# Optimization experiments

Measured on AMD Instinct MI355X. Metric: run time of the kernel, lower is better.

The kernel has to match this reference:

```python
import jax, jax.numpy as jnp
import numpy as np

MIN_STD = 0.01
FOURIER_SCALE = 20.0


def _grid_sample_bilinear(h_flat, gx, gy):
    """Bilinear grid_sample with align_corners=True.
    h_flat: (N, C, H, W); gx, gy: (N, P) in [-1, 1].
    Returns (N, P, C)."""
    N, C, H, W = h_flat.shape
    x = (gx + 1.0) * 0.5 * (W - 1)
    y = (gy + 1.0) * 0.5 * (H - 1)
    x0 = jnp.clip(jnp.floor(x), 0, W - 1)
    y0 = jnp.clip(jnp.floor(y), 0, H - 1)
    x1 = jnp.clip(x0 + 1, 0, W - 1)
    y1 = jnp.clip(y0 + 1, 0, H - 1)
    wx = x - x0
    wy = y - y0
    x0i, x1i = x0.astype(jnp.int32), x1.astype(jnp.int32)
    y0i, y1i = y0.astype(jnp.int32), y1.astype(jnp.int32)
    hf = h_flat.reshape(N, C, H * W)  # flatten spatial for gather

    def gather(yi, xi):
        idx = (yi * W + xi)[:, None, :]  # (N,1,P)
        return jnp.take_along_axis(hf, idx, axis=2)  # (N,C,P)

    v00 = gather(y0i, x0i)
    v01 = gather(y0i, x1i)
    v10 = gather(y1i, x0i)
    v11 = gather(y1i, x1i)
    wx_ = wx[:, None, :]
    wy_ = wy[:, None, :]
    top = v00 * (1 - wx_) + v01 * wx_
    bot = v10 * (1 - wx_) + v11 * wx_
    out = top * (1 - wy_) + bot * wy_  # (N,C,P)
    return out.transpose(0, 2, 1)  # (N,P,C)


def setup_inputs() -> dict:
    key = jax.random.key(0)
    ks = jax.random.split(key, 9)
    B, T, C, Hg, Wg, P = 8, 16, 128, 64, 64, 2048
    h_dim, fmap = 128, 128
    in_dim = h_dim + 2 * fmap  # 384
    h_grid = jax.random.normal(ks[0], (B, T, C, Hg, Wg), dtype=jnp.float32)
    xs = jax.random.uniform(ks[1], (B, T, P, 1), dtype=jnp.float32)
    ys = jax.random.uniform(ks[2], (B, T, P, 1), dtype=jnp.float32)
    B_mat = jax.random.normal(ks[3], (2, fmap), dtype=jnp.float32) * FOURIER_SCALE
    W0 = jax.random.normal(ks[4], (in_dim, h_dim), dtype=jnp.float32) / np.sqrt(in_dim)
    b0 = jnp.zeros((h_dim,), dtype=jnp.float32)
    W1 = jax.random.normal(ks[5], (h_dim, h_dim), dtype=jnp.float32) / np.sqrt(h_dim)
    b1 = jnp.zeros((h_dim,), dtype=jnp.float32)
    W2 = jax.random.normal(ks[6], (h_dim, 2), dtype=jnp.float32) / np.sqrt(h_dim)
    b2 = jnp.zeros((2,), dtype=jnp.float32)
    return {"h_grid": h_grid, "xs": xs, "ys": ys, "B_mat": B_mat,
            "W0": W0, "b0": b0, "W1": W1, "b1": b1, "W2": W2, "b2": b2}


def reference(h_grid, xs, ys, B_mat, W0, b0, W1, b1, W2, b2):
    B, T, P, _ = xs.shape
    _, _, C, Hg, Wg = h_grid.shape
    h_flat = h_grid.reshape(B * T, C, Hg, Wg)
    coords = jnp.concatenate([xs, ys], axis=-1).reshape(B * T, P, 2)
    # map [spatial_min, spatial_max]=[0,1] to [-1,1]
    g = 2.0 * coords - 1.0
    sampled = _grid_sample_bilinear(h_flat, g[..., 0], g[..., 1])  # (BT,P,C)
    # Fourier features: [sin(2pi x B), cos(2pi x B)]
    proj = 2.0 * jnp.pi * jnp.einsum('npd,df->npf', coords, B_mat)
    spatial = jnp.concatenate([jnp.sin(proj), jnp.cos(proj)], axis=-1)  # (BT,P,256)
    x = jnp.concatenate([sampled, spatial], axis=-1)  # (BT,P,384)
    x = jax.nn.relu(x @ W0 + b0)
    x = jax.nn.relu(x @ W1 + b1)
    out = (x @ W2 + b2).reshape(B, T, P, 2)
    mu = out[..., 0:1]
    sigma = jax.nn.softplus(out[..., 1:2]) + MIN_STD
    return jnp.concatenate([mu, sigma], axis=-1)  # (B,T,P,2)
```

## Files before the change

### kernel.cpp

```cpp
#include <hip/hip_runtime.h>
#include <hip/hip_bf16.h>
#include <math.h>

typedef __attribute__((ext_vector_type(8))) short short8;
typedef __attribute__((ext_vector_type(4))) float f32x4;
typedef __attribute__((ext_vector_type(4))) unsigned short us4;

#define MFMA_BF16 __builtin_amdgcn_mfma_f32_16x16x32_bf16

__device__ __forceinline__ float b2f(unsigned short u) {
    union { unsigned int i; float f; } v; v.i = ((unsigned int)u) << 16; return v.f;
}
__device__ __forceinline__ unsigned short f2b(float f) {
    __hip_bfloat16 h = __float2bfloat16(f);
    return *reinterpret_cast<unsigned short*>(&h);
}

__global__ __launch_bounds__(256) void transpose_h(const float* __restrict__ hg,
                                                   unsigned short* __restrict__ ht) {
    __shared__ float t[128][65];
    int bid = blockIdx.x;
    int x = bid & 7, r = bid >> 3;
    int n = x * 16 + (r & 15);
    int pb = r >> 4;
    int tid = threadIdx.x;
    const float* src = hg + (size_t)n * 128 * 4096 + pb * 64;
    int j = tid & 63, i0 = tid >> 6;
#pragma unroll
    for (int ii = 0; ii < 32; ++ii) {
        int ch = ii * 4 + i0;
        t[ch][j] = src[(size_t)ch * 4096 + j];
    }
    __syncthreads();
#pragma unroll
    for (int it = 0; it < 8; ++it) {
        int idx = tid + it * 256;
        int px = idx >> 5, cq = idx & 31;
        us4 o;
#pragma unroll
        for (int rr = 0; rr < 4; ++rr) o[rr] = f2b(t[cq * 4 + rr][px]);
        *(us4*)&ht[((size_t)n * 4096 + pb * 64 + px) * 128 + cq * 4] = o;
    }
}

__global__ void prep_weights(const float* __restrict__ W0, const float* __restrict__ W1,
                             const float* __restrict__ W2,
                             unsigned short* __restrict__ w0t, unsigned short* __restrict__ w1t,
                             unsigned short* __restrict__ w2p) {
    int i = blockIdx.x * 256 + threadIdx.x;
    for (int idx = i; idx < 128 * 384; idx += gridDim.x * 256) {
        int j = idx / 384, k = idx - j * 384;
        w0t[idx] = f2b(W0[k * 128 + j]);
    }
    for (int idx = i; idx < 128 * 128; idx += gridDim.x * 256) {
        int j = idx >> 7, k = idx & 127;
        w1t[idx] = f2b(W1[k * 128 + j]);
    }
    for (int idx = i; idx < 16 * 128; idx += gridDim.x * 256) {
        int r = idx >> 7, k = idx & 127;
        w2p[idx] = (r < 2) ? f2b(W2[k * 2 + r]) : (unsigned short)0;
    }
}

#define W0P 784
#define HBP 272

__global__ __launch_bounds__(512, 2) void fused_decoder(
    const unsigned short* __restrict__ ht,
    const float* __restrict__ xs, const float* __restrict__ ys,
    const float* __restrict__ Bm,
    const unsigned short* __restrict__ w0t, const float* __restrict__ b0,
    const unsigned short* __restrict__ w1t, const float* __restrict__ b1,
    const unsigned short* __restrict__ w2p, const float* __restrict__ b2,
    float* __restrict__ out)
{
    __shared__ char smem[128 * W0P + 8 * 16 * HBP];
    char* w0s = smem;
    int tid = threadIdx.x, lane = tid & 63, w = tid >> 6;
    int lr = lane & 15, lg = lane >> 4;
    char* hb = smem + 128 * W0P + w * 16 * HBP;

    {
        const short8* src = (const short8*)w0t;
#pragma unroll 1
        for (int it = 0; it < 12; ++it) {
            int c = tid + it * 512;
            int row = c / 48, cc = c - row * 48;
            *(short8*)(w0s + row * W0P + cc * 16) = src[c];
        }
    }
    __syncthreads();

    int bid = blockIdx.x;
    int x = bid & 7, s = bid >> 3;
    int n = x * 16 + (s >> 4);
    int pt = s & 15;
    int gp0 = n * 2048 + pt * 128 + w * 16;
    int gp = gp0 + lr;

    float xc = xs[gp], yc = ys[gp];
    float px = xc * 63.f, py = yc * 63.f;
    float x0f = fminf(fmaxf(floorf(px), 0.f), 63.f);
    float y0f = fminf(fmaxf(floorf(py), 0.f), 63.f);
    float wx = px - x0f, wy = py - y0f;
    float ivx = 1.f - wx, ivy = 1.f - wy;
    int xi0 = (int)x0f, yi0 = (int)y0f;
    int xi1 = min(xi0 + 1, 63), yi1 = min(yi0 + 1, 63);
    int o00 = (yi0 * 64 + xi0) * 256, o01 = (yi0 * 64 + xi1) * 256;
    int o10 = (yi1 * 64 + xi0) * 256, o11 = (yi1 * 64 + xi1) * 256;
    const char* base = (const char*)ht + ((size_t)n << 20) + lg * 16;

    f32x4 acc[8];
#pragma unroll
    for (int nj = 0; nj < 8; ++nj) {
        float bv = b0[nj * 16 + lr];
        acc[nj] = (f32x4){bv, bv, bv, bv};
    }

    short8 A00, A01, A10, A11;
    short8 B00, B01, B10, B11;
    A00 = *(const short8*)(base + o00);
    A01 = *(const short8*)(base + o01);
    A10 = *(const short8*)(base + o10);
    A11 = *(const short8*)(base + o11);
    B00 = *(const short8*)(base + o00 + 64);
    B01 = *(const short8*)(base + o01 + 64);
    B10 = *(const short8*)(base + o10 + 64);
    B11 = *(const short8*)(base + o11 + 64);

#pragma unroll 1
    for (int s2 = 0; s2 < 2; ++s2) {
#pragma unroll
        for (int half = 0; half < 2; ++half) {
            int q = 2 * s2 + half;
            short8 asn, acs;
            {
                int f0 = q * 32 + lg * 8;
                f32x4 B0a = *(const f32x4*)&Bm[f0];
                f32x4 B0b = *(const f32x4*)&Bm[f0 + 4];
                f32x4 B1a = *(const f32x4*)&Bm[128 + f0];
                f32x4 B1b = *(const f32x4*)&Bm[128 + f0 + 4];
                float t_[8];
#pragma unroll
                for (int jj = 0; jj < 4; ++jj) {
                    t_[jj]     = xc * B0a[jj] + yc * B1a[jj];
                    t_[4 + jj] = xc * B0b[jj] + yc * B1b[jj];
                }
#pragma unroll
                for (int jj = 0; jj < 8; ++jj) {
                    float tf = t_[jj] - floorf(t_[jj]);
                    float sv, cv;
                    asm("v_sin_f32 %0, %1" : "=v"(sv) : "v"(tf));
                    asm("v_cos_f32 %0, %1" : "=v"(cv) : "v"(tf));
                    asn[jj] = (short)f2b(sv);
                    acs[jj] = (short)f2b(cv);
                }
            }
#pragma unroll
            for (int nj = 0; nj < 8; ++nj) {
                short8 bs = *(const short8*)(w0s + (nj * 16 + lr) * W0P + (4 + q) * 64 + lg * 16);
                acc[nj] = MFMA_BF16(asn, bs, acc[nj], 0, 0, 0);
            }
#pragma unroll
            for (int nj = 0; nj < 8; ++nj) {
                short8 bc = *(const short8*)(w0s + (nj * 16 + lr) * W0P + (8 + q) * 64 + lg * 16);
                acc[nj] = MFMA_BF16(acs, bc, acc[nj], 0, 0, 0);
            }
            short8 a;
            {
                short8 c0 = half ? B00 : A00, c1 = half ? B01 : A01;
                short8 c2 = half ? B10 : A10, c3 = half ? B11 : A11;
#pragma unroll
                for (int jj = 0; jj < 8; ++jj) {
                    float top = b2f((unsigned short)c0[jj]) * ivx + b2f((unsigned short)c1[jj]) * wx;
                    float bot = b2f((unsigned short)c2[jj]) * ivx + b2f((unsigned short)c3[jj]) * wx;
                    a[jj] = (short)f2b(top * ivy + bot * wy);
                }
            }
            if (s2 == 0) {
                int so = (q + 2) * 64;
                if (half == 0) {
                    A00 = *(const short8*)(base + o00 + so);
                    A01 = *(const short8*)(base + o01 + so);
                    A10 = *(const short8*)(base + o10 + so);
                    A11 = *(const short8*)(base + o11 + so);
                } else {
                    B00 = *(const short8*)(base + o00 + so);
                    B01 = *(const short8*)(base + o01 + so);
                    B10 = *(const short8*)(base + o10 + so);
                    B11 = *(const short8*)(base + o11 + so);
                }
            }
#pragma unroll
            for (int nj = 0; nj < 8; ++nj) {
                short8 b = *(const short8*)(w0s + (nj * 16 + lr) * W0P + q * 64 + lg * 16);
                acc[nj] = MFMA_BF16(a, b, acc[nj], 0, 0, 0);
            }
        }
    }

#pragma unroll
    for (int nj = 0; nj < 8; ++nj)
#pragma unroll
        for (int r = 0; r < 4; ++r) {
            int row = lg * 4 + r;
            *(unsigned short*)(hb + row * HBP + (nj * 16 + lr) * 2) =
                f2b(fmaxf(acc[nj][r], 0.f));
        }
    asm volatile("s_waitcnt lgkmcnt(0)" ::: "memory");
    short8 a1[4];
#pragma unroll
    for (int ks = 0; ks < 4; ++ks)
        a1[ks] = *(const short8*)(hb + lr * HBP + ks * 64 + lg * 16);
    asm volatile("s_waitcnt lgkmcnt(0)" ::: "memory");

#pragma unroll
    for (int nj = 0; nj < 8; ++nj) {
        float bv = b1[nj * 16 + lr];
        acc[nj] = (f32x4){bv, bv, bv, bv};
    }
#pragma unroll
    for (int ks = 0; ks < 4; ++ks)
#pragma unroll
        for (int nj = 0; nj < 8; ++nj) {
            short8 b = *(const short8*)&w1t[(nj * 16 + lr) * 128 + ks * 32 + lg * 8];
            acc[nj] = MFMA_BF16(a1[ks], b, acc[nj], 0, 0, 0);
        }

#pragma unroll
    for (int nj = 0; nj < 8; ++nj)
#pragma unroll
        for (int r = 0; r < 4; ++r) {
            int row = lg * 4 + r;
            *(unsigned short*)(hb + row * HBP + (nj * 16 + lr) * 2) =
                f2b(fmaxf(acc[nj][r], 0.f));
        }
    asm volatile("s_waitcnt lgkmcnt(0)" ::: "memory");
    float bb2 = (lr < 2) ? b2[lr] : 0.f;
    f32x4 acc2 = (f32x4){bb2, bb2, bb2, bb2};
#pragma unroll
    for (int ks = 0; ks < 4; ++ks) {
        short8 a2 = *(const short8*)(hb + lr * HBP + ks * 64 + lg * 16);
        short8 bz = *(const short8*)&w2p[lr * 128 + ks * 32 + lg * 8];
        acc2 = MFMA_BF16(a2, bz, acc2, 0, 0, 0);
    }
    asm volatile("s_waitcnt lgkmcnt(0)" ::: "memory");
    if (lr < 2) {
#pragma unroll
        for (int r = 0; r < 4; ++r) {
            int gpo = gp0 + lg * 4 + r;
            float v = acc2[r];
            if (lr == 0) {
                out[gpo * 2] = v;
            } else {
                float sp = (v > 20.f) ? v : log1pf(expf(v));
                out[gpo * 2 + 1] = sp + 0.01f;
            }
        }
    }
}

extern "C" void kernel_launch(void* const* d_in, const int* in_sizes, int n_in,
                              void* d_out, int out_size, void* d_ws, size_t ws_size,
                              hipStream_t stream) {
    const float* h_grid = (const float*)d_in[0];
    const float* xs = (const float*)d_in[1];
    const float* ys = (const float*)d_in[2];
    const float* Bm = (const float*)d_in[3];
    const float* W0 = (const float*)d_in[4];
    const float* b0 = (const float*)d_in[5];
    const float* W1 = (const float*)d_in[6];
    const float* b1 = (const float*)d_in[7];
    const float* W2 = (const float*)d_in[8];
    const float* b2 = (const float*)d_in[9];
    float* out = (float*)d_out;

    unsigned short* ht  = (unsigned short*)d_ws;
    unsigned short* w0t = (unsigned short*)((char*)d_ws + 134217728ull);
    unsigned short* w1t = w0t + 128 * 384;
    unsigned short* w2p = w1t + 128 * 128;

    transpose_h<<<dim3(8192), dim3(256), 0, stream>>>(h_grid, ht);
    prep_weights<<<dim3(64), dim3(256), 0, stream>>>(W0, W1, W2, w0t, w1t, w2p);
    fused_decoder<<<dim3(2048), dim3(512), 0, stream>>>(ht, xs, ys, Bm, w0t, b0, w1t, b1, w2p, b2, out);
}
```

Measured before the change: 240.4 us.

## Use 1024-thread blocks and halve per-wave LDS staging buffer

Result: no change. 242.1 us (+0.7%).

```diff
diff --git a/kernel.cpp b/kernel.cpp
--- a/kernel.cpp
+++ b/kernel.cpp
@@ -63,9 +63,9 @@
 }
 
 #define W0P 784
-#define HBP 272
-
-__global__ __launch_bounds__(512, 2) void fused_decoder(
+#define HBW 144
+
+__global__ __launch_bounds__(1024) void fused_decoder(
     const unsigned short* __restrict__ ht,
     const float* __restrict__ xs, const float* __restrict__ ys,
     const float* __restrict__ Bm,
@@ -74,17 +74,17 @@
     const unsigned short* __restrict__ w2p, const float* __restrict__ b2,
     float* __restrict__ out)
 {
-    __shared__ char smem[128 * W0P + 8 * 16 * HBP];
+    __shared__ char smem[128 * W0P + 16 * 16 * HBW];
     char* w0s = smem;
     int tid = threadIdx.x, lane = tid & 63, w = tid >> 6;
     int lr = lane & 15, lg = lane >> 4;
-    char* hb = smem + 128 * W0P + w * 16 * HBP;
+    char* hb = smem + 128 * W0P + w * 16 * HBW;
 
     {
         const short8* src = (const short8*)w0t;
 #pragma unroll 1
-        for (int it = 0; it < 12; ++it) {
-            int c = tid + it * 512;
+        for (int it = 0; it < 6; ++it) {
+            int c = tid + it * 1024;
             int row = c / 48, cc = c - row * 48;
             *(short8*)(w0s + row * W0P + cc * 16) = src[c];
         }
@@ -93,9 +93,9 @@
 
     int bid = blockIdx.x;
     int x = bid & 7, s = bid >> 3;
-    int n = x * 16 + (s >> 4);
-    int pt = s & 15;
-    int gp0 = n * 2048 + pt * 128 + w * 16;
+    int n = x * 16 + (s >> 3);
+    int pt = s & 7;
+    int gp0 = n * 2048 + pt * 256 + w * 16;
     int gp = gp0 + lr;
 
     float xc = xs[gp], yc = ys[gp];
@@ -199,20 +199,22 @@
         }
     }
 
-#pragma unroll
-    for (int nj = 0; nj < 8; ++nj)
-#pragma unroll
-        for (int r = 0; r < 4; ++r) {
-            int row = lg * 4 + r;
-            *(unsigned short*)(hb + row * HBP + (nj * 16 + lr) * 2) =
-                f2b(fmaxf(acc[nj][r], 0.f));
-        }
-    asm volatile("s_waitcnt lgkmcnt(0)" ::: "memory");
     short8 a1[4];
 #pragma unroll
-    for (int ks = 0; ks < 4; ++ks)
-        a1[ks] = *(const short8*)(hb + lr * HBP + ks * 64 + lg * 16);
-    asm volatile("s_waitcnt lgkmcnt(0)" ::: "memory");
+    for (int hf = 0; hf < 2; ++hf) {
+#pragma unroll
+        for (int nj = 0; nj < 4; ++nj)
+#pragma unroll
+            for (int r = 0; r < 4; ++r) {
+                int row = lg * 4 + r;
+                *(unsigned short*)(hb + row * HBW + (nj * 16 + lr) * 2) =
+                    f2b(fmaxf(acc[hf * 4 + nj][r], 0.f));
+            }
+        asm volatile("s_waitcnt lgkmcnt(0)" ::: "memory");
+        a1[hf * 2]     = *(const short8*)(hb + lr * HBW + lg * 16);
+        a1[hf * 2 + 1] = *(const short8*)(hb + lr * HBW + 64 + lg * 16);
+        asm volatile("s_waitcnt lgkmcnt(0)" ::: "memory");
+    }
 
 #pragma unroll
     for (int nj = 0; nj < 8; ++nj) {
@@ -227,24 +229,28 @@
             acc[nj] = MFMA_BF16(a1[ks], b, acc[nj], 0, 0, 0);
         }
 
-#pragma unroll
-    for (int nj = 0; nj < 8; ++nj)
-#pragma unroll
-        for (int r = 0; r < 4; ++r) {
-            int row = lg * 4 + r;
-            *(unsigned short*)(hb + row * HBP + (nj * 16 + lr) * 2) =
-                f2b(fmaxf(acc[nj][r], 0.f));
-        }
-    asm volatile("s_waitcnt lgkmcnt(0)" ::: "memory");
     float bb2 = (lr < 2) ? b2[lr] : 0.f;
     f32x4 acc2 = (f32x4){bb2, bb2, bb2, bb2};
 #pragma unroll
-    for (int ks = 0; ks < 4; ++ks) {
-        short8 a2 = *(const short8*)(hb + lr * HBP + ks * 64 + lg * 16);
-        short8 bz = *(const short8*)&w2p[lr * 128 + ks * 32 + lg * 8];
-        acc2 = MFMA_BF16(a2, bz, acc2, 0, 0, 0);
-    }
-    asm volatile("s_waitcnt lgkmcnt(0)" ::: "memory");
+    for (int hf = 0; hf < 2; ++hf) {
+#pragma unroll
+        for (int nj = 0; nj < 4; ++nj)
+#pragma unroll
+            for (int r = 0; r < 4; ++r) {
+                int row = lg * 4 + r;
+                *(unsigned short*)(hb + row * HBW + (nj * 16 + lr) * 2) =
+                    f2b(fmaxf(acc[hf * 4 + nj][r], 0.f));
+            }
+        asm volatile("s_waitcnt lgkmcnt(0)" ::: "memory");
+#pragma unroll
+        for (int k2 = 0; k2 < 2; ++k2) {
+            int ks = hf * 2 + k2;
+            short8 a2 = *(const short8*)(hb + lr * HBW + k2 * 64 + lg * 16);
+            short8 bz = *(const short8*)&w2p[lr * 128 + ks * 32 + lg * 8];
+            acc2 = MFMA_BF16(a2, bz, acc2, 0, 0, 0);
+        }
+        asm volatile("s_waitcnt lgkmcnt(0)" ::: "memory");
+    }
     if (lr < 2) {
 #pragma unroll
         for (int r = 0; r < 4; ++r) {
@@ -282,5 +288,5 @@
 
     transpose_h<<<dim3(8192), dim3(256), 0, stream>>>(h_grid, ht);
     prep_weights<<<dim3(64), dim3(256), 0, stream>>>(W0, W1, W2, w0t, w1t, w2p);
-    fused_decoder<<<dim3(2048), dim3(512), 0, stream>>>(ht, xs, ys, Bm, w0t, b0, w1t, b1, w2p, b2, out);
-}
+    fused_decoder<<<dim3(1024), dim3(1024), 0, stream>>>(ht, xs, ys, Bm, w0t, b0, w1t, b1, w2p, b2, out);
+}
```
